# Kernel optimization log

Hardware: AMD Instinct MI355X
Metric: run time of the kernel (lower is better)

The kernel has to match this reference:

```python
import jax, jax.numpy as jnp
import numpy as np
from jax import lax

B, C, H, W = 8, 256, 128, 128


def _scan_along(x, decay, axis):
    """Linear decay recurrence s_t = decay*s_{t-1} + (1-decay)*x_t along `axis`.

    x: [B, C, H, W]; decay: [C] (constant per channel).
    """
    xm = jnp.moveaxis(x, axis, 0)          # [L, B, C, rest]
    d = decay.reshape(1, -1, 1)            # broadcast over [B, C, rest]
    one_minus_d = 1.0 - d

    def step(state, cur):
        state = d * state + one_minus_d * cur
        return state, state

    init = jnp.zeros_like(xm[0])
    _, ys = lax.scan(step, init, xm)
    return jnp.moveaxis(ys, 0, axis)


def setup_inputs() -> dict:
    key = jax.random.key(0)
    k1, k2, k3, k4 = jax.random.split(key, 4)
    x = jax.random.normal(k1, (B, C, H, W), dtype=jnp.float32)
    decay_logits = 0.5 * jax.random.normal(k2, (4, C), dtype=jnp.float32)
    mix_logits = 0.5 * jax.random.normal(k3, (4, C), dtype=jnp.float32)
    input_scale = 0.5 * jax.random.normal(k4, (4, C), dtype=jnp.float32)
    return {"x": x, "decay_logits": decay_logits,
            "mix_logits": mix_logits, "input_scale": input_scale}


def reference(x, decay_logits, mix_logits, input_scale):
    decay = jnp.clip(jax.nn.sigmoid(decay_logits), 0.05, 0.995)   # [4, C]
    mix = jax.nn.softmax(mix_logits, axis=0)                       # [4, C]
    scale = 1.0 + jnp.tanh(input_scale)                            # [4, C]

    def sc(d):  # per-channel [C] -> broadcastable [1, C, 1, 1]
        return d.reshape(1, -1, 1, 1)

    # left -> right: scan along width (axis 3)
    lr = _scan_along(x * sc(scale[0]), decay[0], axis=3)
    # right -> left: flip width, scan, flip back
    rl = jnp.flip(_scan_along(jnp.flip(x, axis=3) * sc(scale[1]), decay[1], axis=3), axis=3)
    # top -> bottom: scan along height (axis 2)
    tb = _scan_along(x * sc(scale[2]), decay[2], axis=2)
    # bottom -> top: flip height, scan, flip back
    bt = jnp.flip(_scan_along(jnp.flip(x, axis=2) * sc(scale[3]), decay[3], axis=2), axis=2)

    return sc(mix[0]) * lr + sc(mix[1]) * rl + sc(mix[2]) * tb + sc(mix[3]) * bt
```

## Files before the change

kernel.cpp:

```cpp
#include <hip/hip_runtime.h>

#define CH 256
#define HH 128
#define WW 128
#define HW (HH * WW)
#define SEGH 16
#define NSEG 8

__device__ __forceinline__ float rdlane(float v, int l) {
    return __int_as_float(__builtin_amdgcn_readlane(__float_as_int(v), l));
}
__device__ __forceinline__ float uni(float v) {
    return __int_as_float(__builtin_amdgcn_readfirstlane(__float_as_int(v)));
}

__global__ __launch_bounds__(1024, 2) void dscan_kernel(
    const float* __restrict__ x,
    const float* __restrict__ decay_logits,
    const float* __restrict__ mix_logits,
    const float* __restrict__ input_scale,
    float* __restrict__ out)
{
    extern __shared__ float smem[];
    float* __restrict__ xs  = smem;
    float* __restrict__ scr = smem + HW;

    const int img  = blockIdx.x;
    const int c    = img & (CH - 1);
    const int tid  = threadIdx.x;
    const int lane = tid & 63;
    const int wv   = tid >> 6;

    float pv = 0.0f;
    {
        const int j = lane & 3;
        const int g = lane >> 2;
        if (g == 0) {
            const float v = decay_logits[j * CH + c];
            pv = fminf(fmaxf(1.0f / (1.0f + expf(-v)), 0.05f), 0.995f);
        } else if (g == 1) {
            const float a0 = mix_logits[0 * CH + c];
            const float a1 = mix_logits[1 * CH + c];
            const float a2 = mix_logits[2 * CH + c];
            const float a3 = mix_logits[3 * CH + c];
            const float mm = fmaxf(fmaxf(a0, a1), fmaxf(a2, a3));
            const float aj = (j == 0) ? a0 : (j == 1) ? a1 : (j == 2) ? a2 : a3;
            pv = expf(aj - mm);
        } else if (g == 2) {
            pv = 1.0f + tanhf(input_scale[j * CH + c]);
        }
    }
    const float d0 = rdlane(pv, 0), d1 = rdlane(pv, 1);
    const float d2 = rdlane(pv, 2), d3 = rdlane(pv, 3);
    const float e0 = rdlane(pv, 4), e1 = rdlane(pv, 5);
    const float e2 = rdlane(pv, 6), e3 = rdlane(pv, 7);
    const float s0 = rdlane(pv, 8), s1 = rdlane(pv, 9);
    const float s2 = rdlane(pv, 10), s3 = rdlane(pv, 11);

    const float einv = uni(1.0f / (e0 + e1 + e2 + e3));
    const float m0 = uni(e0 * einv), m1 = uni(e1 * einv);
    const float m2 = uni(e2 * einv), m3 = uni(e3 * einv);
    const float c0 = uni((1.0f - d0) * s0);
    const float c1 = uni((1.0f - d1) * s1);
    const float c2 = uni((1.0f - d2) * s2);
    const float c3 = uni((1.0f - d3) * s3);

    float q0[5], q1[5];
    q0[0] = uni((d0 * d0) * (d0 * d0));
    q1[0] = uni((d1 * d1) * (d1 * d1));
#pragma unroll
    for (int k = 1; k < 5; ++k) {
        q0[k] = uni(q0[k-1] * q0[k-1]);
        q1[k] = uni(q1[k-1] * q1[k-1]);
    }
    float t2v = d2 * d2; t2v = t2v * t2v; t2v = t2v * t2v; const float d2p16 = uni(t2v * t2v);
    float t3v = d3 * d3; t3v = t3v * t3v; t3v = t3v * t3v; const float d3p16 = uni(t3v * t3v);

    const float* __restrict__ xg = x + (size_t)img * HW;
    float* __restrict__ og = out + (size_t)img * HW;

    {
        const int sl   = lane & 31;
        const int half = lane >> 5;
        const int rbase = (wv << 1) + half;

        float4 v[4];
#pragma unroll
        for (int it = 0; it < 4; ++it)
            v[it] = *(const float4*)(xg + ((it << 5) + rbase) * WW + (sl << 2));

#pragma unroll
        for (int it = 0; it < 4; ++it) {
            const int r = (it << 5) + rbase;
            const float4 xv4 = v[it];

            float bL = c0 * xv4.x;
            bL = fmaf(d0, bL, c0 * xv4.y);
            bL = fmaf(d0, bL, c0 * xv4.z);
            bL = fmaf(d0, bL, c0 * xv4.w);
            float bR = c1 * xv4.w;
            bR = fmaf(d1, bR, c1 * xv4.z);
            bR = fmaf(d1, bR, c1 * xv4.y);
            bR = fmaf(d1, bR, c1 * xv4.x);

#pragma unroll
            for (int k = 0; k < 5; ++k) {
                const int off = 1 << k;
                const float bU = __shfl_up(bL, (unsigned)off, 32);
                bL = fmaf(q0[k], (sl >= off) ? bU : 0.0f, bL);
                const float bD = __shfl_down(bR, (unsigned)off, 32);
                bR = fmaf(q1[k], (sl < 32 - off) ? bD : 0.0f, bR);
            }
            float EL = __shfl_up(bL, 1u, 32);
            if (sl == 0) EL = 0.0f;
            float ER = __shfl_down(bR, 1u, 32);
            if (sl == 31) ER = 0.0f;

            const float l0 = fmaf(d0, EL, c0 * xv4.x);
            const float l1 = fmaf(d0, l0, c0 * xv4.y);
            const float l2 = fmaf(d0, l1, c0 * xv4.z);
            const float l3 = fmaf(d0, l2, c0 * xv4.w);
            const float r3 = fmaf(d1, ER, c1 * xv4.w);
            const float r2 = fmaf(d1, r3, c1 * xv4.z);
            const float r1 = fmaf(d1, r2, c1 * xv4.y);
            const float r0 = fmaf(d1, r1, c1 * xv4.x);

            float4 o4;
            o4.x = fmaf(m0, l0, m1 * r0);
            o4.y = fmaf(m0, l1, m1 * r1);
            o4.z = fmaf(m0, l2, m1 * r2);
            o4.w = fmaf(m0, l3, m1 * r3);
            *(float4*)(xs + r * WW + (sl << 2)) = o4;
        }
    }

    const int col = tid & (WW - 1);
    const int seg = tid >> 7;
    const float* __restrict__ xcol = xg + seg * SEGH * WW + col;

    float xv[SEGH];
    {
#pragma unroll
        for (int i = 0; i < SEGH; ++i) xv[i] = xcol[i * WW];

        float b2 = 0.0f;
#pragma unroll
        for (int i = 0; i < SEGH; ++i) b2 = fmaf(d2, b2, c2 * xv[i]);

        float b3 = 0.0f;
#pragma unroll
        for (int i = SEGH - 1; i >= 0; --i) b3 = fmaf(d3, b3, xv[i]);
        b3 *= c3;

        scr[tid]        = b2;
        scr[1024 + tid] = b3;
    }

    __syncthreads();

    float Sin = 0.0f;
    for (int j = 0; j < seg; ++j)
        Sin = fmaf(d2p16, Sin, scr[j * WW + col]);
    float Tin = 0.0f;
    for (int j = NSEG - 1; j > seg; --j)
        Tin = fmaf(d3p16, Tin, scr[1024 + j * WW + col]);

    {
        float* __restrict__ pcol = xs + seg * SEGH * WW + col;
        float* __restrict__ ocol = og + seg * SEGH * WW + col;

        float s = Sin;
#pragma unroll
        for (int i = 0; i < SEGH; ++i) {
            s = fmaf(d2, s, c2 * xv[i]);
            pcol[i * WW] = fmaf(m2, s, pcol[i * WW]);
        }
        float t = Tin;
#pragma unroll
        for (int i = SEGH - 1; i >= 0; --i) {
            t = fmaf(d3, t, c3 * xv[i]);
            ocol[i * WW] = fmaf(m3, t, pcol[i * WW]);
        }
    }
}

extern "C" void kernel_launch(void* const* d_in, const int* in_sizes, int n_in,
                              void* d_out, int out_size, void* d_ws, size_t ws_size,
                              hipStream_t stream) {
    const float* x  = (const float*)d_in[0];
    const float* dl = (const float*)d_in[1];
    const float* ml = (const float*)d_in[2];
    const float* is = (const float*)d_in[3];
    float* out = (float*)d_out;

    const size_t lds_bytes = (size_t)(HW + 2048) * sizeof(float);

    static bool attr_set = false;
    if (!attr_set) {
        (void)hipFuncSetAttribute((const void*)dscan_kernel,
                                  hipFuncAttributeMaxDynamicSharedMemorySize,
                                  (int)lds_bytes);
        attr_set = true;
    }

    dim3 grid(2048), block(1024);
    hipLaunchKernelGGL(dscan_kernel, grid, block, lds_bytes, stream, x, dl, ml, is, out);
}
```

Before: 239.3 us.

## Use 16-element per-thread row scans with 8-lane shuffles and swizzled LDS

Each thread now runs the horizontal scan over a 16-element row chunk, with 8 threads per row. This replaces the 4-element chunks that needed 32-lane shuffle prefix steps, cutting the shuffle steps from 5 to 3. The row results are stored to LDS with an XOR swizzle, and the vertical pass reads them with the matching swizzle to reduce bank conflicts. The vertical pass also buffers its outputs in registers instead of doing a read-modify-write to LDS. The cost is more registers per thread, under the 1024-thread launch bound.

```diff
diff --git a/kernel.cpp b/kernel.cpp
--- a/kernel.cpp
+++ b/kernel.cpp
@@ -29,7 +29,6 @@
     const int c    = img & (CH - 1);
     const int tid  = threadIdx.x;
     const int lane = tid & 63;
-    const int wv   = tid >> 6;
 
     float pv = 0.0f;
     {
@@ -65,13 +64,12 @@
     const float c2 = uni((1.0f - d2) * s2);
     const float c3 = uni((1.0f - d3) * s3);
 
-    float q0[5], q1[5];
-    q0[0] = uni((d0 * d0) * (d0 * d0));
-    q1[0] = uni((d1 * d1) * (d1 * d1));
-#pragma unroll
-    for (int k = 1; k < 5; ++k) {
-        q0[k] = uni(q0[k-1] * q0[k-1]);
-        q1[k] = uni(q1[k-1] * q1[k-1]);
+    float q0[3], q1[3];
+    {
+        float a = d0 * d0; a = a * a; a = a * a; a = a * a;
+        q0[0] = uni(a); q0[1] = uni(q0[0] * q0[0]); q0[2] = uni(q0[1] * q0[1]);
+        float b = d1 * d1; b = b * b; b = b * b; b = b * b;
+        q1[0] = uni(b); q1[1] = uni(q1[0] * q1[0]); q1[2] = uni(q1[1] * q1[1]);
     }
     float t2v = d2 * d2; t2v = t2v * t2v; t2v = t2v * t2v; const float d2p16 = uni(t2v * t2v);
     float t3v = d3 * d3; t3v = t3v * t3v; t3v = t3v * t3v; const float d3p16 = uni(t3v * t3v);
@@ -80,57 +78,56 @@
     float* __restrict__ og = out + (size_t)img * HW;
 
     {
-        const int sl   = lane & 31;
-        const int half = lane >> 5;
-        const int rbase = (wv << 1) + half;
-
-        float4 v[4];
-#pragma unroll
-        for (int it = 0; it < 4; ++it)
-            v[it] = *(const float4*)(xg + ((it << 5) + rbase) * WW + (sl << 2));
-
-#pragma unroll
-        for (int it = 0; it < 4; ++it) {
-            const int r = (it << 5) + rbase;
-            const float4 xv4 = v[it];
-
-            float bL = c0 * xv4.x;
-            bL = fmaf(d0, bL, c0 * xv4.y);
-            bL = fmaf(d0, bL, c0 * xv4.z);
-            bL = fmaf(d0, bL, c0 * xv4.w);
-            float bR = c1 * xv4.w;
-            bR = fmaf(d1, bR, c1 * xv4.z);
-            bR = fmaf(d1, bR, c1 * xv4.y);
-            bR = fmaf(d1, bR, c1 * xv4.x);
-
-#pragma unroll
-            for (int k = 0; k < 5; ++k) {
-                const int off = 1 << k;
-                const float bU = __shfl_up(bL, (unsigned)off, 32);
-                bL = fmaf(q0[k], (sl >= off) ? bU : 0.0f, bL);
-                const float bD = __shfl_down(bR, (unsigned)off, 32);
-                bR = fmaf(q1[k], (sl < 32 - off) ? bD : 0.0f, bR);
-            }
-            float EL = __shfl_up(bL, 1u, 32);
-            if (sl == 0) EL = 0.0f;
-            float ER = __shfl_down(bR, 1u, 32);
-            if (sl == 31) ER = 0.0f;
-
-            const float l0 = fmaf(d0, EL, c0 * xv4.x);
-            const float l1 = fmaf(d0, l0, c0 * xv4.y);
-            const float l2 = fmaf(d0, l1, c0 * xv4.z);
-            const float l3 = fmaf(d0, l2, c0 * xv4.w);
-            const float r3 = fmaf(d1, ER, c1 * xv4.w);
-            const float r2 = fmaf(d1, r3, c1 * xv4.z);
-            const float r1 = fmaf(d1, r2, c1 * xv4.y);
-            const float r0 = fmaf(d1, r1, c1 * xv4.x);
-
+        const int hr = tid >> 3;
+        const int hk = tid & 7;
+
+        const float* __restrict__ xrow = xg + hr * WW + hk * 16;
+        const float4 a0 = *(const float4*)(xrow + 0);
+        const float4 a1 = *(const float4*)(xrow + 4);
+        const float4 a2 = *(const float4*)(xrow + 8);
+        const float4 a3 = *(const float4*)(xrow + 12);
+        float xr[16];
+        xr[0]=a0.x;  xr[1]=a0.y;  xr[2]=a0.z;  xr[3]=a0.w;
+        xr[4]=a1.x;  xr[5]=a1.y;  xr[6]=a1.z;  xr[7]=a1.w;
+        xr[8]=a2.x;  xr[9]=a2.y;  xr[10]=a2.z; xr[11]=a2.w;
+        xr[12]=a3.x; xr[13]=a3.y; xr[14]=a3.z; xr[15]=a3.w;
+
+        float bL = c0 * xr[0];
+#pragma unroll
+        for (int i = 1; i < 16; ++i) bL = fmaf(d0, bL, c0 * xr[i]);
+        float bR = c1 * xr[15];
+#pragma unroll
+        for (int i = 14; i >= 0; --i) bR = fmaf(d1, bR, c1 * xr[i]);
+
+#pragma unroll
+        for (int kk = 0; kk < 3; ++kk) {
+            const int off = 1 << kk;
+            const float bU = __shfl_up(bL, (unsigned)off, 8);
+            bL = fmaf(q0[kk], (hk >= off) ? bU : 0.0f, bL);
+            const float bD = __shfl_down(bR, (unsigned)off, 8);
+            bR = fmaf(q1[kk], (hk < 8 - off) ? bD : 0.0f, bR);
+        }
+        float EL = __shfl_up(bL, 1u, 8);
+        if (hk == 0) EL = 0.0f;
+        float ER = __shfl_down(bR, 1u, 8);
+        if (hk == 7) ER = 0.0f;
+
+        float rr[16];
+        float t = ER;
+#pragma unroll
+        for (int i = 15; i >= 0; --i) { t = fmaf(d1, t, c1 * xr[i]); rr[i] = t; }
+
+        float l = EL;
+        float* __restrict__ prow = xs + hr * WW + hk * 16;
+        const int rsw = hr & 3;
+#pragma unroll
+        for (int j = 0; j < 4; ++j) {
             float4 o4;
-            o4.x = fmaf(m0, l0, m1 * r0);
-            o4.y = fmaf(m0, l1, m1 * r1);
-            o4.z = fmaf(m0, l2, m1 * r2);
-            o4.w = fmaf(m0, l3, m1 * r3);
-            *(float4*)(xs + r * WW + (sl << 2)) = o4;
+            l = fmaf(d0, l, c0 * xr[4*j + 0]); o4.x = fmaf(m0, l, m1 * rr[4*j + 0]);
+            l = fmaf(d0, l, c0 * xr[4*j + 1]); o4.y = fmaf(m0, l, m1 * rr[4*j + 1]);
+            l = fmaf(d0, l, c0 * xr[4*j + 2]); o4.z = fmaf(m0, l, m1 * rr[4*j + 2]);
+            l = fmaf(d0, l, c0 * xr[4*j + 3]); o4.w = fmaf(m0, l, m1 * rr[4*j + 3]);
+            *(float4*)(prow + 4 * (j ^ rsw)) = o4;
         }
     }
 
@@ -139,10 +136,10 @@
     const float* __restrict__ xcol = xg + seg * SEGH * WW + col;
 
     float xv[SEGH];
-    {
-#pragma unroll
-        for (int i = 0; i < SEGH; ++i) xv[i] = xcol[i * WW];
-
+#pragma unroll
+    for (int i = 0; i < SEGH; ++i) xv[i] = xcol[i * WW];
+
+    {
         float b2 = 0.0f;
 #pragma unroll
         for (int i = 0; i < SEGH; ++i) b2 = fmaf(d2, b2, c2 * xv[i]);
@@ -166,20 +163,21 @@
         Tin = fmaf(d3p16, Tin, scr[1024 + j * WW + col]);
 
     {
-        float* __restrict__ pcol = xs + seg * SEGH * WW + col;
-        float* __restrict__ ocol = og + seg * SEGH * WW + col;
-
+        const int rbase = seg * SEGH;
+        float o[SEGH];
         float s = Sin;
 #pragma unroll
         for (int i = 0; i < SEGH; ++i) {
             s = fmaf(d2, s, c2 * xv[i]);
-            pcol[i * WW] = fmaf(m2, s, pcol[i * WW]);
+            const float h = xs[(rbase + i) * WW + (col ^ ((i & 3) << 2))];
+            o[i] = fmaf(m2, s, h);
         }
         float t = Tin;
+        float* __restrict__ ocol = og + rbase * WW + col;
 #pragma unroll
         for (int i = SEGH - 1; i >= 0; --i) {
             t = fmaf(d3, t, c3 * xv[i]);
-            ocol[i * WW] = fmaf(m3, t, pcol[i * WW]);
+            ocol[i * WW] = fmaf(m3, t, o[i]);
         }
     }
 }
```

After: 242.2 us. Within noise of the previous version (+1.2%).
